# Performance work log

Hardware: AMD Instinct MI355X
Metric: run time of the kernel (lower is better)

## Reference

```python
import jax, jax.numpy as jnp
import numpy as np

HEAD_DIM = 32
KS = 3            # kernel_size
DIL = 2           # dilation
PAD = DIL * (KS - 1) // 2
SCALE = HEAD_DIM ** (-0.5)


def _unfold(x):
    """nn.ReflectionPad2d(PAD) + nn.Unfold(KS, dilation=DIL).
    x: [B, C, H, W] -> [B, C, KS*KS, H, W] with kernel positions row-major,
    matching nn.Unfold's (C, kh, kw) channel ordering."""
    B, C, H, W = x.shape
    xp = jnp.pad(x, ((0, 0), (0, 0), (PAD, PAD), (PAD, PAD)), mode='reflect')
    patches = jnp.stack(
        [xp[:, :, i * DIL:i * DIL + H, j * DIL:j * DIL + W]
         for i in range(KS) for j in range(KS)],
        axis=2,
    )
    return patches  # [B, C, ksq, H, W]


def setup_inputs() -> dict:
    key = jax.random.key(0)
    kq, kk, kv = jax.random.split(key, 3)
    shape = (16, 384, 56, 56)
    return {
        'q': jax.random.normal(kq, shape, dtype=jnp.float32),
        'k': jax.random.normal(kk, shape, dtype=jnp.float32),
        'v': jax.random.normal(kv, shape, dtype=jnp.float32),
    }


def reference(q, k, v):
    B, d, H, W = q.shape
    nH = d // HEAD_DIM
    ksq = KS * KS
    # q: [B, nH, headDim, H, W]
    q_r = q.reshape(B, nH, HEAD_DIM, H, W)
    # k/v unfolded: [B, nH, headDim, ksq, H, W]
    k_p = _unfold(k).reshape(B, nH, HEAD_DIM, ksq, H, W)
    v_p = _unfold(v).reshape(B, nH, HEAD_DIM, ksq, H, W)
    # attention scores over the ksq local window
    attn = jnp.einsum('bnchw,bnckhw->bnkhw', q_r, k_p) * SCALE
    attn = jax.nn.softmax(attn, axis=2)
    out = jnp.einsum('bnkhw,bnckhw->bnchw', attn, v_p)
    # [B, nH, headDim, H, W] -> [B, H, W, nH*headDim]
    out = out.reshape(B, d, H, W).transpose(0, 2, 3, 1)
    return out
```

## Files before the change

### kernel.cpp

```cpp
#include <hip/hip_runtime.h>
#include <stdint.h>


#define BB 16
#define CH 384
#define HH 56
#define WW 56
#define NH 12
#define DD 32
#define HW (HH * WW)
#define KSQ 9
#define SCALE 0.17677669529663687f

#define BAND 8
#define DCH 8
#define NCHUNK (DD / DCH)
#define MAXROWS 12
#define SLICE (MAXROWS * WW)
#define LBUF (DCH * SLICE)

#define WAITV(n) asm volatile("s_waitcnt vmcnt(" #n ")" ::: "memory")
#define FENCE()  asm volatile("" ::: "memory")
#define BAR()    do { FENCE(); __builtin_amdgcn_s_barrier(); FENCE(); } while (0)

__device__ __forceinline__ void async16(const void* g, void* l) {
    __builtin_amdgcn_global_load_lds(
        (const __attribute__((address_space(1))) void*)g,
        (__attribute__((address_space(3))) void*)l, 16, 0, 0);
}

__device__ __forceinline__ void stage_chunk(const float* __restrict__ plane0,
                                            float* ldsbuf, int Sbytes,
                                            int wv, int lane) {
    const int lo16 = lane * 16;
    const char* g = (const char*)(plane0 + wv * HW);
    char* l = (char*)(ldsbuf + wv * SLICE);
    async16(g + lo16, l + lo16);
    async16(g + 1024 + lo16, l + 1024 + lo16);
    const int t = Sbytes - 1024;
    async16(g + t + lo16, l + t + lo16);
}

__global__ __launch_bounds__(512, 6)
void dilate_attn_kernel(const float* __restrict__ q,
                        const float* __restrict__ k,
                        const float* __restrict__ v,
                        float* __restrict__ out) {
    __shared__ __align__(16) float lds[2][LBUF];

    const int band = blockIdx.x;
    const int n    = blockIdx.y;
    const int b    = blockIdx.z;

    const int tid  = threadIdx.x;
    const int lane = tid & 63;
    const int wv   = tid >> 6;

    const bool act = lane < WW;
    const int w  = act ? lane : (WW - 1);
    const int h0 = band * BAND;
    const int h  = h0 + wv;

    const int lo = (h0 - 2 < 0) ? 0 : h0 - 2;
    const int hi = (h0 + 9 > HH - 1) ? HH - 1 : h0 + 9;
    const int Sbytes = (hi - lo + 1) * WW * 4;

    int off9[KSQ];
    {
        int wc[3];
#pragma unroll
        for (int j = 0; j < 3; ++j) {
            int c = w + 2 * (j - 1);
            c = (c < 0) ? -c : ((c >= WW) ? (2 * WW - 2 - c) : c);
            wc[j] = c;
        }
#pragma unroll
        for (int i = 0; i < 3; ++i) {
            int rr = h + 2 * (i - 1);
            rr = (rr < 0) ? -rr : ((rr >= HH) ? (2 * HH - 2 - rr) : rr);
            rr -= lo;
#pragma unroll
            for (int j = 0; j < 3; ++j) off9[i * 3 + j] = rr * WW + wc[j];
        }
    }

    const int planebase = (b * CH + n * DD) * HW;
    const float* qp = q + planebase + h * WW + w;
    const float* kstage = k + planebase + lo * WW;
    const float* vstage = v + planebase + lo * WW;

    float sc[KSQ];
#pragma unroll
    for (int ii = 0; ii < KSQ; ++ii) sc[ii] = 0.f;

    stage_chunk(kstage, lds[0], Sbytes, wv, lane);
    FENCE();
    float qd[DCH];
#pragma unroll
    for (int j = 0; j < DCH; ++j) qd[j] = qp[j * HW];
    FENCE();
    stage_chunk(kstage + DCH * HW, lds[1], Sbytes, wv, lane);
    FENCE();

#pragma unroll
    for (int c = 0; c < NCHUNK; ++c) {
        WAITV(11);
        BAR();
        float qn[DCH];
        if (c < NCHUNK - 1) {
#pragma unroll
            for (int j = 0; j < DCH; ++j) qn[j] = qp[((c + 1) * DCH + j) * HW];
        }
        const float* Bf = lds[c & 1];
#pragma unroll
        for (int j = 0; j < DCH; ++j) {
            const float* Ls = Bf + j * SLICE;
            const float qj = qd[j];
#pragma unroll
            for (int ii = 0; ii < KSQ; ++ii)
                sc[ii] = fmaf(qj, Ls[off9[ii]], sc[ii]);
        }
        if (c < NCHUNK - 1) {
#pragma unroll
            for (int j = 0; j < DCH; ++j) qd[j] = qn[j];
        }
        BAR();
        const float* src = (c + 2 < NCHUNK)
                               ? (kstage + (c + 2) * DCH * HW)
                               : (vstage + (c + 2 - NCHUNK) * DCH * HW);
        stage_chunk(src, lds[c & 1], Sbytes, wv, lane);
        FENCE();
    }

    {
        float m = sc[0];
#pragma unroll
        for (int ii = 1; ii < KSQ; ++ii) m = fmaxf(m, sc[ii]);
        float sum = 0.f;
#pragma unroll
        for (int ii = 0; ii < KSQ; ++ii) {
            sc[ii] = __expf((sc[ii] - m) * SCALE);
            sum += sc[ii];
        }
        const float inv = 1.f / sum;
#pragma unroll
        for (int ii = 0; ii < KSQ; ++ii) sc[ii] *= inv;
    }

    float* op = out + ((b * HH + h) * WW + w) * CH + n * DD;

#pragma unroll
    for (int p = 0; p < NCHUNK; ++p) {
        if (p == 0)      WAITV(3);
        else if (p == 3) WAITV(2);
        else             WAITV(5);
        BAR();
        const float* Bf = lds[p & 1];
        float o[DCH];
#pragma unroll
        for (int j = 0; j < DCH; ++j) {
            const float* Ls = Bf + j * SLICE;
            float acc = 0.f;
#pragma unroll
            for (int ii = 0; ii < KSQ; ++ii)
                acc = fmaf(sc[ii], Ls[off9[ii]], acc);
            o[j] = acc;
        }
        if (act) {
            *(float4*)(op + p * DCH)     = make_float4(o[0], o[1], o[2], o[3]);
            *(float4*)(op + p * DCH + 4) = make_float4(o[4], o[5], o[6], o[7]);
        }
        if (p < 2) {
            BAR();
            stage_chunk(vstage + (p + 2) * DCH * HW, lds[p & 1], Sbytes, wv, lane);
            FENCE();
        }
    }
}

extern "C" void kernel_launch(void* const* d_in, const int* in_sizes, int n_in,
                              void* d_out, int out_size, void* d_ws, size_t ws_size,
                              hipStream_t stream) {
    const float* q = (const float*)d_in[0];
    const float* k = (const float*)d_in[1];
    const float* v = (const float*)d_in[2];
    float* out = (float*)d_out;

    dim3 grid(HH / BAND, NH, BB);
    dilate_attn_kernel<<<grid, 512, 0, stream>>>(q, k, v, out);
}
```

Baseline: 276.9 us.

## Stage K/V chunks through registers instead of async global-to-LDS loads

Replaces the direct global_load_lds async copies with ordinary float4 global loads into a two-deep register ring, followed by explicit LDS stores plus an lgkmcnt wait and barrier. The loop now issues the chunk-ahead global load before the compute and writes the next chunk into LDS after it, so the hand-tuned vmcnt accounting goes away. This costs extra VGPRs (six float4) and an additional barrier per chunk, which may hurt occupancy under the 512x6 launch bound. It also adds explicit LDS write instructions in exchange for simpler compiler-visible dependencies.

Result: slower. 371.0 us (+34.0%).

```diff
diff --git a/kernel.cpp b/kernel.cpp
--- a/kernel.cpp
+++ b/kernel.cpp
@@ -19,26 +19,24 @@
 #define SLICE (MAXROWS * WW)
 #define LBUF (DCH * SLICE)
 
-#define WAITV(n) asm volatile("s_waitcnt vmcnt(" #n ")" ::: "memory")
 #define FENCE()  asm volatile("" ::: "memory")
 #define BAR()    do { FENCE(); __builtin_amdgcn_s_barrier(); FENCE(); } while (0)
+#define LGKM0()  asm volatile("s_waitcnt lgkmcnt(0)" ::: "memory")
 
-__device__ __forceinline__ void async16(const void* g, void* l) {
-    __builtin_amdgcn_global_load_lds(
-        (const __attribute__((address_space(1))) void*)g,
-        (__attribute__((address_space(3))) void*)l, 16, 0, 0);
+__device__ __forceinline__ void ldg3(const float* __restrict__ plane0,
+                                     int Sbytes, int wv, int lane, float4* r) {
+    const char* g = (const char*)(plane0 + wv * HW) + lane * 16;
+    r[0] = *(const float4*)(g);
+    r[1] = *(const float4*)(g + 1024);
+    r[2] = *(const float4*)(g + (Sbytes - 1024));
 }
 
-__device__ __forceinline__ void stage_chunk(const float* __restrict__ plane0,
-                                            float* ldsbuf, int Sbytes,
-                                            int wv, int lane) {
-    const int lo16 = lane * 16;
-    const char* g = (const char*)(plane0 + wv * HW);
-    char* l = (char*)(ldsbuf + wv * SLICE);
-    async16(g + lo16, l + lo16);
-    async16(g + 1024 + lo16, l + 1024 + lo16);
-    const int t = Sbytes - 1024;
-    async16(g + t + lo16, l + t + lo16);
+__device__ __forceinline__ void dsw3(float* ldsbuf, int Sbytes, int wv,
+                                     int lane, const float4* r) {
+    char* l = (char*)(ldsbuf + wv * SLICE) + lane * 16;
+    *(float4*)(l) = r[0];
+    *(float4*)(l + 1024) = r[1];
+    *(float4*)(l + (Sbytes - 1024)) = r[2];
 }
 
 __global__ __launch_bounds__(512, 6)
@@ -93,19 +91,27 @@
 #pragma unroll
     for (int ii = 0; ii < KSQ; ++ii) sc[ii] = 0.f;
 
-    stage_chunk(kstage, lds[0], Sbytes, wv, lane);
+    float4 S[2][3];
+
+    ldg3(kstage, Sbytes, wv, lane, S[0]);
+    FENCE();
+    ldg3(kstage + DCH * HW, Sbytes, wv, lane, S[1]);
     FENCE();
     float qd[DCH];
 #pragma unroll
     for (int j = 0; j < DCH; ++j) qd[j] = qp[j * HW];
     FENCE();
-    stage_chunk(kstage + DCH * HW, lds[1], Sbytes, wv, lane);
-    FENCE();
+    dsw3(lds[0], Sbytes, wv, lane, S[0]);
+    LGKM0();
+    BAR();
 
 #pragma unroll
     for (int c = 0; c < NCHUNK; ++c) {
-        WAITV(11);
-        BAR();
+        const float* src = (c + 2 < NCHUNK)
+                               ? (kstage + (c + 2) * DCH * HW)
+                               : (vstage + (c + 2 - NCHUNK) * DCH * HW);
+        ldg3(src, Sbytes, wv, lane, S[c & 1]);
+        FENCE();
         float qn[DCH];
         if (c < NCHUNK - 1) {
 #pragma unroll
@@ -125,11 +131,9 @@
             for (int j = 0; j < DCH; ++j) qd[j] = qn[j];
         }
         BAR();
-        const float* src = (c + 2 < NCHUNK)
-                               ? (kstage + (c + 2) * DCH * HW)
-                               : (vstage + (c + 2 - NCHUNK) * DCH * HW);
-        stage_chunk(src, lds[c & 1], Sbytes, wv, lane);
-        FENCE();
+        dsw3(lds[(c + 1) & 1], Sbytes, wv, lane, S[(c + 1) & 1]);
+        LGKM0();
+        BAR();
     }
 
     {
@@ -151,10 +155,10 @@
 
 #pragma unroll
     for (int p = 0; p < NCHUNK; ++p) {
-        if (p == 0)      WAITV(3);
-        else if (p == 3) WAITV(2);
-        else             WAITV(5);
-        BAR();
+        if (p + 2 < NCHUNK) {
+            ldg3(vstage + (p + 2) * DCH * HW, Sbytes, wv, lane, S[p & 1]);
+            FENCE();
+        }
         const float* Bf = lds[p & 1];
         float o[DCH];
 #pragma unroll
@@ -170,10 +174,11 @@
             *(float4*)(op + p * DCH)     = make_float4(o[0], o[1], o[2], o[3]);
             *(float4*)(op + p * DCH + 4) = make_float4(o[4], o[5], o[6], o[7]);
         }
-        if (p < 2) {
+        if (p < NCHUNK - 1) {
             BAR();
-            stage_chunk(vstage + (p + 2) * DCH * HW, lds[p & 1], Sbytes, wv, lane);
-            FENCE();
+            dsw3(lds[(p + 1) & 1], Sbytes, wv, lane, S[(p + 1) & 1]);
+            LGKM0();
+            BAR();
         }
     }
 }
```
